# Kernel optimization log

Measured on AMD Instinct MI355X. Metric: run time of the kernel, lower is better.

Reference implementation:

```python
import jax, jax.numpy as jnp
import numpy as np

N_HEAD = 12
M_HIST = 5      # Anderson history window (AndersonAcceleration.m)
BETA = 1.0      # Anderson mixing (AndersonAcceleration.beta)
LN_EPS = 1e-5


def _layer_norm(x, w, b):
    mu = x.mean(-1, keepdims=True)
    xc = x - mu
    var = (xc * xc).mean(-1, keepdims=True)
    return xc * jax.lax.rsqrt(var + LN_EPS) * w + b


def _mha(x, wqkv, bqkv, wo, bo):
    # torch nn.MultiheadAttention, batch_first, self-attention, no mask, dropout=0
    B, T, C = x.shape
    dh = C // N_HEAD
    qkv = x @ wqkv.T + bqkv                       # [B,T,3C]
    q, k, v = jnp.split(qkv, 3, axis=-1)
    def heads(t):
        return t.reshape(B, T, N_HEAD, dh).transpose(0, 2, 1, 3)  # [B,H,T,dh]
    q, k, v = heads(q), heads(k), heads(v)
    scores = jnp.einsum('bhqd,bhkd->bhqk', q, k) / jnp.sqrt(jnp.asarray(dh, x.dtype))
    att = jax.nn.softmax(scores, axis=-1)
    out = jnp.einsum('bhqk,bhkd->bhqd', att, v).transpose(0, 2, 1, 3).reshape(B, T, C)
    return out @ wo.T + bo


def _deq_delta(z, u, emb_row, ln1_w, ln1_b, in_proj_w, in_proj_b, out_proj_w,
               out_proj_b, ln2_w, ln2_b, mlp_w1, mlp_b1, mlp_w2, mlp_b2):
    # DEQOperator.forward -> delta_z
    z_temporal = z + 0.1 * emb_row                 # broadcast [C] over [B,T,C]
    z_ctx = z_temporal + u
    x = _layer_norm(z_ctx, ln1_w, ln1_b)
    attn_out = _mha(x, in_proj_w, in_proj_b, out_proj_w, out_proj_b)
    z_attn = z + attn_out
    h = _layer_norm(z_attn, ln2_w, ln2_b)
    h = jax.nn.gelu(h @ mlp_w1.T + mlp_b1, approximate=False) @ mlp_w2.T + mlp_b2
    z_mlp = z_attn + h
    return z_mlp - z


def _deq_solve(u, iter_emb, ln1_w, ln1_b, in_proj_w, in_proj_b, out_proj_w,
               out_proj_b, ln2_w, ln2_b, mlp_w1, mlp_b1, mlp_w2, mlp_b2, num_iters):
    B, T, C = u.shape
    z = jnp.zeros_like(u)
    Xs, Fs = [], []   # Anderson history of states / residuals
    max_row = iter_emb.shape[0] - 1
    for it in range(num_iters):
        emb_row = iter_emb[min(it, max_row)]
        delta = _deq_delta(z, u, emb_row, ln1_w, ln1_b, in_proj_w, in_proj_b,
                           out_proj_w, out_proj_b, ln2_w, ln2_b,
                           mlp_w1, mlp_b1, mlp_w2, mlp_b2)
        res = delta  # residual of f(z) = z + delta_z w.r.t. z
        Xs.append(z); Fs.append(res)
        if len(Xs) > M_HIST:
            Xs.pop(0); Fs.pop(0)
        if len(Xs) == 1:
            z = z + BETA * res
        else:
            K = len(Xs) - 1
            dF = jnp.stack(Fs[:-1], 0) - res[None]               # [K,B,T,C]
            dF_f = dF.transpose(1, 2, 0, 3).reshape(B * T, K, C)  # per-token LS
            r_f = res.reshape(B * T, C)
            G = jnp.einsum('nkc,nlc->nkl', dF_f, dF_f)            # [BT,K,K]
            G = G + 1e-6 * jnp.eye(K, dtype=u.dtype)
            bvec = jnp.einsum('nkc,nc->nk', dF_f, r_f)            # [BT,K]
            alpha = jnp.linalg.solve(G, bvec[..., None])[..., 0]
            d = r_f - jnp.einsum('nkc,nk->nc', dF_f, alpha)
            z = (z.reshape(B * T, C) + BETA * d).reshape(B, T, C)
    return z


def setup_inputs() -> dict:
    key = jax.random.key(0)
    ks = jax.random.split(key, 6)
    B, T, C = 4, 1024, 768
    std = 0.02
    return {
        'u': jax.random.normal(ks[0], (B, T, C), jnp.float32),
        'iter_emb': std * jax.random.normal(ks[1], (31, C), jnp.float32),
        'ln1_w': jnp.ones((C,), jnp.float32),
        'ln1_b': jnp.zeros((C,), jnp.float32),
        'in_proj_w': std * jax.random.normal(ks[2], (3 * C, C), jnp.float32),
        'in_proj_b': jnp.zeros((3 * C,), jnp.float32),
        'out_proj_w': std * jax.random.normal(ks[3], (C, C), jnp.float32),
        'out_proj_b': jnp.zeros((C,), jnp.float32),
        'ln2_w': jnp.ones((C,), jnp.float32),
        'ln2_b': jnp.zeros((C,), jnp.float32),
        'mlp_w1': std * jax.random.normal(ks[4], (4 * C, C), jnp.float32),
        'mlp_b1': jnp.zeros((4 * C,), jnp.float32),
        'mlp_w2': std * jax.random.normal(ks[5], (C, 4 * C), jnp.float32),
        'mlp_b2': jnp.zeros((C,), jnp.float32),
        'num_iters': 6,
    }


def reference(u, iter_emb, ln1_w, ln1_b, in_proj_w, in_proj_b, out_proj_w,
              out_proj_b, ln2_w, ln2_b, mlp_w1, mlp_b1, mlp_w2, mlp_b2, num_iters):
    return _deq_solve(u, iter_emb, ln1_w, ln1_b, in_proj_w, in_proj_b,
                      out_proj_w, out_proj_b, ln2_w, ln2_b,
                      mlp_w1, mlp_b1, mlp_w2, mlp_b2, int(num_iters))
```

## Files before the change

kernel.cpp:

```cpp
#include <hip/hip_runtime.h>
#include <math.h>

#define BT 4096
#define CDIM 768
#define NHEAD 12
#define DH 64
#define TSEQ 1024
#define BBATCH 4

typedef _Float16 f16;
typedef __attribute__((ext_vector_type(4))) _Float16 f16x4;
typedef __attribute__((ext_vector_type(8))) _Float16 f16x8;
typedef __attribute__((ext_vector_type(4))) float f32x4;

typedef const __attribute__((address_space(1))) unsigned int* gas1_t;
typedef __attribute__((address_space(3))) unsigned int* las3_t;
__device__ __forceinline__ void glds16(const void* g, void* l) {
  __builtin_amdgcn_global_load_lds((gas1_t)g, (las3_t)l, 16, 0, 0);
}

__device__ __forceinline__ float block_reduce_sum(float v, float* sbuf) {
#pragma unroll
  for (int o = 32; o > 0; o >>= 1) v += __shfl_down(v, o, 64);
  int lane = threadIdx.x & 63;
  int w = threadIdx.x >> 6;
  if (lane == 0) sbuf[w] = v;
  __syncthreads();
  float r = sbuf[0] + sbuf[1] + sbuf[2] + sbuf[3];
  __syncthreads();
  return r;
}

__global__ __launch_bounds__(256) void zero_kernel(float4* __restrict__ p) {
  p[(size_t)blockIdx.x * 256 + threadIdx.x] = make_float4(0.f, 0.f, 0.f, 0.f);
}

__global__ __launch_bounds__(256) void cvt_f16_kernel(
    const float* __restrict__ in, f16* __restrict__ out) {
  size_t i = ((size_t)blockIdx.x * 256 + threadIdx.x) * 4;
  float4 v = *(const float4*)(in + i);
  f16x4 o = {(f16)v.x, (f16)v.y, (f16)v.z, (f16)v.w};
  *(f16x4*)(out + i) = o;
}

__global__ __launch_bounds__(256) void ln1_kernel(
    const float* __restrict__ z, const float* __restrict__ u,
    const float* __restrict__ emb, const float* __restrict__ w,
    const float* __restrict__ b, f16* __restrict__ x) {
  __shared__ float sbuf[4];
  int row = blockIdx.x;
  int tid = threadIdx.x;
  const float* zr = z + (size_t)row * CDIM;
  const float* ur = u + (size_t)row * CDIM;
  float v[3];
  float s = 0.f;
#pragma unroll
  for (int i = 0; i < 3; i++) {
    int c = tid + i * 256;
    v[i] = zr[c] + 0.1f * emb[c] + ur[c];
    s += v[i];
  }
  s = block_reduce_sum(s, sbuf);
  float mu = s * (1.f / CDIM);
  float sq = 0.f;
#pragma unroll
  for (int i = 0; i < 3; i++) { v[i] -= mu; sq += v[i] * v[i]; }
  sq = block_reduce_sum(sq, sbuf);
  float rstd = rsqrtf(sq * (1.f / CDIM) + 1e-5f);
  f16* xr = x + (size_t)row * CDIM;
#pragma unroll
  for (int i = 0; i < 3; i++) {
    int c = tid + i * 256;
    xr[c] = (f16)(v[i] * rstd * w[c] + b[c]);
  }
}

__global__ __launch_bounds__(256) void ln2_kernel(
    const float* __restrict__ in, const float* __restrict__ w,
    const float* __restrict__ b, f16* __restrict__ x,
    const float* __restrict__ z, const float* __restrict__ b2,
    float* __restrict__ rinit) {
  __shared__ float sbuf[4];
  int row = blockIdx.x;
  int tid = threadIdx.x;
  const float* ir = in + (size_t)row * CDIM;
  const float* zr = z + (size_t)row * CDIM;
  float* rr = rinit + (size_t)row * CDIM;
  float v[3];
  float s = 0.f;
#pragma unroll
  for (int i = 0; i < 3; i++) {
    int c = tid + i * 256;
    v[i] = ir[c];
    rr[c] = v[i] - zr[c] + b2[c];
    s += v[i];
  }
  s = block_reduce_sum(s, sbuf);
  float mu = s * (1.f / CDIM);
  float sq = 0.f;
#pragma unroll
  for (int i = 0; i < 3; i++) { v[i] -= mu; sq += v[i] * v[i]; }
  sq = block_reduce_sum(sq, sbuf);
  float rstd = rsqrtf(sq * (1.f / CDIM) + 1e-5f);
  f16* xr = x + (size_t)row * CDIM;
#pragma unroll
  for (int i = 0; i < 3; i++) {
    int c = tid + i * 256;
    xr[c] = (f16)(v[i] * rstd * w[c] + b[c]);
  }
}

__device__ __forceinline__ float gelu_exact(float t) {
  return 0.5f * t * (1.f + erff(t * 0.70710678118654752f));
}

template <int MODE>
__global__ __launch_bounds__(256, 3) void gemm_mfma(
    const f16* __restrict__ A, const f16* __restrict__ W,
    const float* __restrict__ bias, f16* __restrict__ hq,
    f16* __restrict__ hk, f16* __restrict__ hvt, f16* __restrict__ hout,
    int M, int N, int K) {
  __shared__ __align__(16) f16 As[128 * 64];
  __shared__ __align__(16) f16 Bs[128 * 64];
  int tid = threadIdx.x;
  int wv = tid >> 6, lane = tid & 63;
  int bm = blockIdx.y, bn = blockIdx.x;
  int wm = (wv >> 1) * 64, wn = (wv & 1) * 64;

  int srow = wv * 32 + (lane >> 3);
  int scole = 8 * ((lane & 7) ^ (lane >> 3));
  const f16* gA = A + (size_t)(bm * 128 + srow) * K + scole;
  const f16* gB = W + (size_t)(bn * 128 + srow) * K + scole;

  f32x4 acc[4][4];
#pragma unroll
  for (int i = 0; i < 4; i++)
#pragma unroll
    for (int j = 0; j < 4; j++) acc[i][j] = (f32x4){0.f, 0.f, 0.f, 0.f};

  int am = lane & 15;
  int quad = lane >> 4;
  int sx = am & 7;

  for (int k0 = 0; k0 < K; k0 += 64) {
    __syncthreads();
#pragma unroll
    for (int j = 0; j < 4; j++) {
      glds16(gA + (size_t)(j * 8) * K + k0, &As[(wv * 32 + j * 8) * 64]);
      glds16(gB + (size_t)(j * 8) * K + k0, &Bs[(wv * 32 + j * 8) * 64]);
    }
    __syncthreads();
#pragma unroll
    for (int kk = 0; kk < 2; kk++) {
      int ce = 8 * (((kk << 2) + quad) ^ sx);
      f16x8 af[4], bfr[4];
#pragma unroll
      for (int mi = 0; mi < 4; mi++)
        af[mi] = *(const f16x8*)&As[(wm + mi * 16 + am) * 64 + ce];
#pragma unroll
      for (int nj = 0; nj < 4; nj++)
        bfr[nj] = *(const f16x8*)&Bs[(wn + nj * 16 + am) * 64 + ce];
#pragma unroll
      for (int mi = 0; mi < 4; mi++)
#pragma unroll
        for (int nj = 0; nj < 4; nj++)
          acc[mi][nj] = __builtin_amdgcn_mfma_f32_16x16x32_f16(
              af[mi], bfr[nj], acc[mi][nj], 0, 0, 0);
    }
  }

  int crow0 = bm * 128 + wm + quad * 4;
  int ccol0 = bn * 128 + wn + am;
#pragma unroll
  for (int nj = 0; nj < 4; nj++) {
    int col = ccol0 + nj * 16;
    float bcol = bias[col];
    if constexpr (MODE == 3) {
      int which = col / CDIM;
      int rem = col - which * CDIM;
      int h = rem >> 6;
      int d = rem & 63;
#pragma unroll
      for (int mi = 0; mi < 4; mi++) {
#pragma unroll
        for (int r = 0; r < 4; r++) {
          int m = crow0 + mi * 16 + r;
          int bb = m >> 10, t = m & 1023;
          f16 val = (f16)(acc[mi][nj][r] + bcol);
          if (which == 0)
            hq[(((size_t)(bb * NHEAD + h) * TSEQ + t) << 6) + d] = val;
          else if (which == 1)
            hk[(((size_t)(bb * NHEAD + h) * TSEQ + t) << 6) + d] = val;
          else
            hvt[(((size_t)(bb * NHEAD + h) * DH + d) << 10) + t] = val;
        }
      }
    } else {
#pragma unroll
      for (int mi = 0; mi < 4; mi++) {
#pragma unroll
        for (int r = 0; r < 4; r++) {
          int m = crow0 + mi * 16 + r;
          size_t idx = (size_t)m * N + col;
          hout[idx] = (f16)gelu_exact(acc[mi][nj][r] + bcol);
        }
      }
    }
  }
}

#define GS 72
template <int MODE>
__global__ __launch_bounds__(256, (MODE == 4) ? 6 : 4) void gemm_mfma64(
    const f16* __restrict__ A, const f16* __restrict__ W,
    const float* __restrict__ bias, const float* __restrict__ aux1,
    float* __restrict__ fout0, int M, int N, int K) {
  __shared__ __align__(16) f16 As[64 * GS];
  __shared__ __align__(16) f16 Bs[64 * GS];
  int tid = threadIdx.x;
  int wv = tid >> 6, lane = tid & 63;
  int bm = blockIdx.x, bn = blockIdx.y;
  int wm = (wv >> 1) * 32, wn = (wv & 1) * 32;

  int ks = (MODE == 4) ? blockIdx.z : 0;
  int kl = (MODE == 4) ? (K >> 1) : K;

  int srow = tid >> 2;
  int scol = (tid & 3) * 16;
  const f16* gA = A + (size_t)(bm * 64 + srow) * K + ks * kl + scol;
  const f16* gB = W + (size_t)(bn * 64 + srow) * K + ks * kl + scol;

  f32x4 acc[2][2];
#pragma unroll
  for (int i = 0; i < 2; i++)
#pragma unroll
    for (int j = 0; j < 2; j++) acc[i][j] = (f32x4){0.f, 0.f, 0.f, 0.f};

  int am = lane & 15;
  int ak = (lane >> 4) * 8;

  f16x8 a0 = *(const f16x8*)(gA);
  f16x8 a1 = *(const f16x8*)(gA + 8);
  f16x8 b0 = *(const f16x8*)(gB);
  f16x8 b1 = *(const f16x8*)(gB + 8);

  for (int k0 = 0; k0 < kl; k0 += 64) {
    __syncthreads();
    *(f16x8*)&As[srow * GS + scol] = a0;
    *(f16x8*)&As[srow * GS + scol + 8] = a1;
    *(f16x8*)&Bs[srow * GS + scol] = b0;
    *(f16x8*)&Bs[srow * GS + scol + 8] = b1;
    __syncthreads();
    int kn = k0 + 64;
    if (kn < kl) {
      a0 = *(const f16x8*)(gA + kn);
      a1 = *(const f16x8*)(gA + kn + 8);
      b0 = *(const f16x8*)(gB + kn);
      b1 = *(const f16x8*)(gB + kn + 8);
    }
#pragma unroll
    for (int kk = 0; kk < 2; kk++) {
      f16x8 af[2], bfr[2];
#pragma unroll
      for (int mi = 0; mi < 2; mi++)
        af[mi] = *(const f16x8*)&As[(wm + mi * 16 + am) * GS + kk * 32 + ak];
#pragma unroll
      for (int nj = 0; nj < 2; nj++)
        bfr[nj] = *(const f16x8*)&Bs[(wn + nj * 16 + am) * GS + kk * 32 + ak];
#pragma unroll
      for (int mi = 0; mi < 2; mi++)
#pragma unroll
        for (int nj = 0; nj < 2; nj++)
          acc[mi][nj] = __builtin_amdgcn_mfma_f32_16x16x32_f16(
              af[mi], bfr[nj], acc[mi][nj], 0, 0, 0);
    }
  }

  int crow0 = bm * 64 + wm + (lane >> 4) * 4;
  int ccol0 = bn * 64 + wn + (lane & 15);
#pragma unroll
  for (int nj = 0; nj < 2; nj++) {
    int col = ccol0 + nj * 16;
    float bcol = (MODE == 4) ? 0.f : bias[col];
#pragma unroll
    for (int mi = 0; mi < 2; mi++) {
#pragma unroll
      for (int r = 0; r < 4; r++) {
        int m = crow0 + mi * 16 + r;
        size_t idx = (size_t)m * N + col;
        if constexpr (MODE == 0) {
          fout0[idx] = acc[mi][nj][r] + bcol + aux1[idx];
        } else {
          unsafeAtomicAdd(fout0 + idx, acc[mi][nj][r]);
        }
      }
    }
  }
}

#define PSTRIDE 72
#define KVS 72
__global__ __launch_bounds__(256, 3) void flash_attn8(
    const f16* __restrict__ Qg, const f16* __restrict__ Kg,
    const f16* __restrict__ Vt, f16* __restrict__ attn) {
  __shared__ __align__(16) f16 Ks[64 * KVS];
  __shared__ __align__(16) f16 Vs[64 * KVS];
  __shared__ __align__(16) f16 Plds[4][16 * PSTRIDE];
  int tid = threadIdx.x;
  int wv = tid >> 6, lane = tid & 63;
  int bh = blockIdx.x;
  int bb = bh / NHEAD, h = bh % NHEAD;
  int m0 = (blockIdx.y * 4 + wv) * 16;
  int am = lane & 15;
  int quad = lane >> 4;
  int ak = quad * 8;

  int srow = tid >> 3;
  int scol = (tid & 7) * 8;

  const f16* kb = Kg + (((size_t)bh * TSEQ) << 6);
  const f16* vb = Vt + (((size_t)bh * DH) << 10);

  const f16* qbase = Qg + (((size_t)bh * TSEQ + m0) << 6);
  f16x8 qf0 = *(const f16x8*)(qbase + am * 64 + ak);
  f16x8 qf1 = *(const f16x8*)(qbase + am * 64 + 32 + ak);
#pragma unroll
  for (int i = 0; i < 8; i++) { qf0[i] *= (f16)0.125f; qf1[i] *= (f16)0.125f; }

  f16* Pw = Plds[wv];
  f32x4 Oa[4];
#pragma unroll
  for (int i = 0; i < 4; i++) Oa[i] = (f32x4){0.f, 0.f, 0.f, 0.f};
  float lpart[4] = {0.f, 0.f, 0.f, 0.f};

  f16x8 kr0 = *(const f16x8*)(kb + (size_t)srow * 64 + scol);
  f16x8 kr1 = *(const f16x8*)(kb + (size_t)(32 + srow) * 64 + scol);
  f16x8 vr0 = *(const f16x8*)(vb + (size_t)srow * TSEQ + scol);
  f16x8 vr1 = *(const f16x8*)(vb + (size_t)(32 + srow) * TSEQ + scol);

  for (int n0 = 0; n0 < TSEQ; n0 += 64) {
    __syncthreads();
    *(f16x8*)&Ks[srow * KVS + scol] = kr0;
    *(f16x8*)&Ks[(32 + srow) * KVS + scol] = kr1;
    *(f16x8*)&Vs[srow * KVS + scol] = vr0;
    *(f16x8*)&Vs[(32 + srow) * KVS + scol] = vr1;
    __syncthreads();
    int nn = n0 + 64;
    if (nn < TSEQ) {
      kr0 = *(const f16x8*)(kb + (size_t)(nn + srow) * 64 + scol);
      kr1 = *(const f16x8*)(kb + (size_t)(nn + 32 + srow) * 64 + scol);
      vr0 = *(const f16x8*)(vb + (size_t)srow * TSEQ + nn + scol);
      vr1 = *(const f16x8*)(vb + (size_t)(32 + srow) * TSEQ + nn + scol);
    }
    f32x4 S[4];
#pragma unroll
    for (int t = 0; t < 4; t++) {
      f16x8 kf0 = *(const f16x8*)&Ks[(16 * t + am) * KVS + ak];
      f16x8 kf1 = *(const f16x8*)&Ks[(16 * t + am) * KVS + 32 + ak];
      S[t] = __builtin_amdgcn_mfma_f32_16x16x32_f16(
          qf0, kf0, (f32x4){0.f, 0.f, 0.f, 0.f}, 0, 0, 0);
      S[t] = __builtin_amdgcn_mfma_f32_16x16x32_f16(qf1, kf1, S[t], 0, 0, 0);
    }
#pragma unroll
    for (int t = 0; t < 4; t++) {
#pragma unroll
      for (int r = 0; r < 4; r++) {
        float p = __expf(S[t][r]);
        lpart[r] += p;
        Pw[(quad * 4 + r) * PSTRIDE + 16 * t + am] = (f16)p;
      }
    }
    f16x8 pa0 = *(const f16x8*)&Pw[am * PSTRIDE + ak];
    f16x8 pa1 = *(const f16x8*)&Pw[am * PSTRIDE + 32 + ak];
#pragma unroll
    for (int dt = 0; dt < 4; dt++) {
      f16x8 vf0 = *(const f16x8*)&Vs[(16 * dt + am) * KVS + ak];
      f16x8 vf1 = *(const f16x8*)&Vs[(16 * dt + am) * KVS + 32 + ak];
      Oa[dt] = __builtin_amdgcn_mfma_f32_16x16x32_f16(pa0, vf0, Oa[dt], 0, 0, 0);
      Oa[dt] = __builtin_amdgcn_mfma_f32_16x16x32_f16(pa1, vf1, Oa[dt], 0, 0, 0);
    }
  }

#pragma unroll
  for (int o = 1; o < 16; o <<= 1)
#pragma unroll
    for (int r = 0; r < 4; r++) lpart[r] += __shfl_xor(lpart[r], o, 64);

#pragma unroll
  for (int r = 0; r < 4; r++) {
    int m = m0 + quad * 4 + r;
    float inv = 1.f / lpart[r];
    f16* orow = attn + ((size_t)(bb * TSEQ + m)) * CDIM + h * DH;
#pragma unroll
    for (int dt = 0; dt < 4; dt++)
      orow[dt * 16 + am] = (f16)(Oa[dt][r] * inv);
  }
}

template <int KA>
__global__ __launch_bounds__(256) void anderson_ln1(
    float* __restrict__ z, const float* __restrict__ rescur,
    const float* __restrict__ p0, const float* __restrict__ p1,
    const float* __restrict__ p2, const float* __restrict__ p3,
    const float* __restrict__ u, const float* __restrict__ emb,
    const float* __restrict__ w, const float* __restrict__ b,
    f16* __restrict__ x) {
  __shared__ float sbuf[4];
  int row = blockIdx.x, tid = threadIdx.x;
  size_t base = (size_t)row * CDIM + tid;
  float r[3];
#pragma unroll
  for (int i = 0; i < 3; i++) r[i] = rescur[base + i * 256];

  float zn[3];
  if constexpr (KA == 0) {
#pragma unroll
    for (int i = 0; i < 3; i++) zn[i] = z[base + i * 256] + r[i];
  } else {
    const float* ps[4] = {p0, p1, p2, p3};
    float dF[KA == 0 ? 1 : KA][3];
#pragma unroll
    for (int k = 0; k < KA; k++)
#pragma unroll
      for (int i = 0; i < 3; i++) dF[k][i] = ps[k][base + i * 256] - r[i];

    float Gm[KA == 0 ? 1 : KA][KA == 0 ? 1 : KA], bv[KA == 0 ? 1 : KA];
#pragma unroll
    for (int k = 0; k < KA; k++) {
#pragma unroll
      for (int ll = k; ll < KA; ll++) {
        float p = 0.f;
#pragma unroll
        for (int i = 0; i < 3; i++) p += dF[k][i] * dF[ll][i];
        float t = block_reduce_sum(p, sbuf);
        Gm[k][ll] = t;
        Gm[ll][k] = t;
      }
    }
#pragma unroll
    for (int k = 0; k < KA; k++) Gm[k][k] += 1e-6f;
#pragma unroll
    for (int k = 0; k < KA; k++) {
      float p = 0.f;
#pragma unroll
      for (int i = 0; i < 3; i++) p += dF[k][i] * r[i];
      bv[k] = block_reduce_sum(p, sbuf);
    }
    float alpha[KA == 0 ? 1 : KA];
#pragma unroll
    for (int p = 0; p < KA; p++) {
      float inv = 1.f / Gm[p][p];
#pragma unroll
      for (int rr = p + 1; rr < KA; rr++) {
        float f = Gm[rr][p] * inv;
#pragma unroll
        for (int c = p; c < KA; c++) Gm[rr][c] -= f * Gm[p][c];
        bv[rr] -= f * bv[p];
      }
    }
#pragma unroll
    for (int p = KA - 1; p >= 0; p--) {
      float s2 = bv[p];
#pragma unroll
      for (int c = p + 1; c < KA; c++) s2 -= Gm[p][c] * alpha[c];
      alpha[p] = s2 / Gm[p][p];
    }
#pragma unroll
    for (int i = 0; i < 3; i++) {
      float d = r[i];
#pragma unroll
      for (int k = 0; k < KA; k++) d = fmaf(-dF[k][i], alpha[k], d);
      zn[i] = z[base + i * 256] + d;
    }
  }
#pragma unroll
  for (int i = 0; i < 3; i++) z[base + i * 256] = zn[i];

  const float* ur = u + (size_t)row * CDIM;
  float v[3];
  float s = 0.f;
#pragma unroll
  for (int i = 0; i < 3; i++) {
    int c = tid + i * 256;
    v[i] = zn[i] + 0.1f * emb[c] + ur[c];
    s += v[i];
  }
  s = block_reduce_sum(s, sbuf);
  float mu = s * (1.f / CDIM);
  float sq = 0.f;
#pragma unroll
  for (int i = 0; i < 3; i++) { v[i] -= mu; sq += v[i] * v[i]; }
  sq = block_reduce_sum(sq, sbuf);
  float rstd = rsqrtf(sq * (1.f / CDIM) + 1e-5f);
  f16* xr = x + (size_t)row * CDIM;
#pragma unroll
  for (int i = 0; i < 3; i++) {
    int c = tid + i * 256;
    xr[c] = (f16)(v[i] * rstd * w[c] + b[c]);
  }
}

template <int KA>
__global__ __launch_bounds__(256) void anderson_kernel(
    float* __restrict__ z, const float* __restrict__ rescur,
    const float* __restrict__ p0, const float* __restrict__ p1,
    const float* __restrict__ p2, const float* __restrict__ p3) {
  __shared__ float sbuf[4];
  int row = blockIdx.x, tid = threadIdx.x;
  size_t base = (size_t)row * CDIM + tid;
  float r[3];
#pragma unroll
  for (int i = 0; i < 3; i++) r[i] = rescur[base + i * 256];
  const float* ps[4] = {p0, p1, p2, p3};
  float dF[KA][3];
#pragma unroll
  for (int k = 0; k < KA; k++)
#pragma unroll
    for (int i = 0; i < 3; i++) dF[k][i] = ps[k][base + i * 256] - r[i];

  float Gm[KA][KA], bv[KA];
#pragma unroll
  for (int k = 0; k < KA; k++) {
#pragma unroll
    for (int ll = k; ll < KA; ll++) {
      float p = 0.f;
#pragma unroll
      for (int i = 0; i < 3; i++) p += dF[k][i] * dF[ll][i];
      float t = block_reduce_sum(p, sbuf);
      Gm[k][ll] = t;
      Gm[ll][k] = t;
    }
  }
#pragma unroll
  for (int k = 0; k < KA; k++) Gm[k][k] += 1e-6f;
#pragma unroll
  for (int k = 0; k < KA; k++) {
    float p = 0.f;
#pragma unroll
    for (int i = 0; i < 3; i++) p += dF[k][i] * r[i];
    bv[k] = block_reduce_sum(p, sbuf);
  }
  float alpha[KA];
#pragma unroll
  for (int p = 0; p < KA; p++) {
    float inv = 1.f / Gm[p][p];
#pragma unroll
    for (int rr = p + 1; rr < KA; rr++) {
      float f = Gm[rr][p] * inv;
#pragma unroll
      for (int c = p; c < KA; c++) Gm[rr][c] -= f * Gm[p][c];
      bv[rr] -= f * bv[p];
    }
  }
#pragma unroll
  for (int p = KA - 1; p >= 0; p--) {
    float s2 = bv[p];
#pragma unroll
    for (int c = p + 1; c < KA; c++) s2 -= Gm[p][c] * alpha[c];
    alpha[p] = s2 / Gm[p][p];
  }
#pragma unroll
  for (int i = 0; i < 3; i++) {
    float d = r[i];
#pragma unroll
    for (int k = 0; k < KA; k++) d = fmaf(-dF[k][i], alpha[k], d);
    z[base + i * 256] += d;
  }
}

extern "C" void kernel_launch(void* const* d_in, const int* in_sizes, int n_in,
                              void* d_out, int out_size, void* d_ws,
                              size_t ws_size, hipStream_t stream) {
  (void)in_sizes; (void)n_in; (void)out_size; (void)ws_size;
  const float* u = (const float*)d_in[0];
  const float* iter_emb = (const float*)d_in[1];
  const float* ln1w = (const float*)d_in[2];
  const float* ln1b = (const float*)d_in[3];
  const float* wqkv = (const float*)d_in[4];
  const float* bqkv = (const float*)d_in[5];
  const float* wo = (const float*)d_in[6];
  const float* bo = (const float*)d_in[7];
  const float* ln2w = (const float*)d_in[8];
  const float* ln2b = (const float*)d_in[9];
  const float* w1 = (const float*)d_in[10];
  const float* b1 = (const float*)d_in[11];
  const float* w2 = (const float*)d_in[12];
  const float* b2 = (const float*)d_in[13];

  const size_t S = (size_t)BT * CDIM;
  float* ws = (float*)d_ws;
  float* z = ws + 0 * S;
  float* zattn = ws + 1 * S;
  float* res[5] = {ws + 2 * S, ws + 3 * S, ws + 4 * S, ws + 5 * S, ws + 6 * S};
  f16* q_h = (f16*)(ws + 7 * S);
  f16* k_h = q_h + S;
  f16* vt_h = q_h + 2 * S;
  f16* h_h = (f16*)(ws + 7 * S);
  f16* x_h = (f16*)(ws + 9 * S);
  f16* wqkv_h = x_h + S;
  f16* wo_h = wqkv_h + (size_t)3 * CDIM * CDIM;
  f16* w1_h = wo_h + (size_t)CDIM * CDIM;
  f16* w2_h = w1_h + (size_t)4 * CDIM * CDIM;

  cvt_f16_kernel<<<1728, 256, 0, stream>>>(wqkv, wqkv_h);
  cvt_f16_kernel<<<576, 256, 0, stream>>>(wo, wo_h);
  cvt_f16_kernel<<<2304, 256, 0, stream>>>(w1, w1_h);
  cvt_f16_kernel<<<2304, 256, 0, stream>>>(w2, w2_h);
  zero_kernel<<<S / 1024, 256, 0, stream>>>((float4*)z);

  for (int it = 0; it < 6; it++) {
    float* rcur = res[it % 5];
    if (it == 0) {
      ln1_kernel<<<BT, 256, 0, stream>>>(z, u, iter_emb, ln1w, ln1b, x_h);
    }
    gemm_mfma<3><<<dim3(18, 32), 256, 0, stream>>>(
        x_h, wqkv_h, bqkv, q_h, k_h, vt_h, nullptr, BT, 3 * CDIM, CDIM);
    flash_attn8<<<dim3(BBATCH * NHEAD, TSEQ / 64), 256, 0, stream>>>(
        q_h, k_h, vt_h, x_h);
    gemm_mfma64<0><<<dim3(64, 12), 256, 0, stream>>>(
        x_h, wo_h, bo, z, zattn, BT, CDIM, CDIM);
    ln2_kernel<<<BT, 256, 0, stream>>>(zattn, ln2w, ln2b, x_h, z, b2, rcur);
    gemm_mfma<1><<<dim3(24, 32), 256, 0, stream>>>(
        x_h, w1_h, b1, nullptr, nullptr, nullptr, h_h, BT, 4 * CDIM, CDIM);
    gemm_mfma64<4><<<dim3(64, 12, 2), 256, 0, stream>>>(
        h_h, w2_h, b2, nullptr, rcur, BT, CDIM, 4 * CDIM);

    int Kh = it < 4 ? it : 4;
    const float* p[4] = {rcur, rcur, rcur, rcur};
    for (int kx = 1; kx <= Kh; kx++) p[kx - 1] = res[(it - kx) % 5];
    if (it < 5) {
      const float* embn = iter_emb + (it + 1) * CDIM;
      switch (Kh) {
        case 0: anderson_ln1<0><<<BT, 256, 0, stream>>>(z, rcur, p[0], p[1], p[2], p[3], u, embn, ln1w, ln1b, x_h); break;
        case 1: anderson_ln1<1><<<BT, 256, 0, stream>>>(z, rcur, p[0], p[1], p[2], p[3], u, embn, ln1w, ln1b, x_h); break;
        case 2: anderson_ln1<2><<<BT, 256, 0, stream>>>(z, rcur, p[0], p[1], p[2], p[3], u, embn, ln1w, ln1b, x_h); break;
        case 3: anderson_ln1<3><<<BT, 256, 0, stream>>>(z, rcur, p[0], p[1], p[2], p[3], u, embn, ln1w, ln1b, x_h); break;
        default: anderson_ln1<4><<<BT, 256, 0, stream>>>(z, rcur, p[0], p[1], p[2], p[3], u, embn, ln1w, ln1b, x_h); break;
      }
    } else {
      anderson_kernel<4><<<BT, 256, 0, stream>>>(z, rcur, p[0], p[1], p[2], p[3]);
    }
  }
  hipMemcpyAsync(d_out, z, S * sizeof(float), hipMemcpyDeviceToDevice, stream);
}
```

Before: 1.150 ms.

## Replace MLP down-projection with 128x128 split-K GEMM using direct global-to-LDS loads

```diff
diff --git a/kernel.cpp b/kernel.cpp
--- a/kernel.cpp
+++ b/kernel.cpp
@@ -209,9 +209,83 @@
   }
 }
 
+#define KCHUNK 768
+__global__ __launch_bounds__(256, 3) void gemm_splitk_glds(
+    const f16* __restrict__ A, const f16* __restrict__ W,
+    float* __restrict__ out, int N, int Ktot) {
+  __shared__ __align__(16) f16 As[128 * 64];
+  __shared__ __align__(16) f16 Bs[128 * 64];
+  int b = blockIdx.x;
+  int n = (b & 7) * 96 + (b >> 3);
+  int bn = n % 6;
+  int bm = (n / 6) & 31;
+  int ks = n / 192;
+
+  int tid = threadIdx.x;
+  int wv = tid >> 6, lane = tid & 63;
+  int wm = (wv >> 1) * 64, wn = (wv & 1) * 64;
+
+  int srow = wv * 32 + (lane >> 3);
+  int scole = 8 * ((lane & 7) ^ (lane >> 3));
+  const f16* gA = A + (size_t)(bm * 128 + srow) * Ktot + ks * KCHUNK + scole;
+  const f16* gB = W + (size_t)(bn * 128 + srow) * Ktot + ks * KCHUNK + scole;
+
+  f32x4 acc[4][4];
+#pragma unroll
+  for (int i = 0; i < 4; i++)
+#pragma unroll
+    for (int j = 0; j < 4; j++) acc[i][j] = (f32x4){0.f, 0.f, 0.f, 0.f};
+
+  int am = lane & 15;
+  int quad = lane >> 4;
+  int sx = am & 7;
+
+  for (int k0 = 0; k0 < KCHUNK; k0 += 64) {
+    __syncthreads();
+#pragma unroll
+    for (int j = 0; j < 4; j++) {
+      glds16(gA + (size_t)(j * 8) * Ktot + k0, &As[(wv * 32 + j * 8) * 64]);
+      glds16(gB + (size_t)(j * 8) * Ktot + k0, &Bs[(wv * 32 + j * 8) * 64]);
+    }
+    __syncthreads();
+#pragma unroll
+    for (int kk = 0; kk < 2; kk++) {
+      int ce = 8 * (((kk << 2) + quad) ^ sx);
+      f16x8 af[4], bfr[4];
+#pragma unroll
+      for (int mi = 0; mi < 4; mi++)
+        af[mi] = *(const f16x8*)&As[(wm + mi * 16 + am) * 64 + ce];
+#pragma unroll
+      for (int nj = 0; nj < 4; nj++)
+        bfr[nj] = *(const f16x8*)&Bs[(wn + nj * 16 + am) * 64 + ce];
+#pragma unroll
+      for (int mi = 0; mi < 4; mi++)
+#pragma unroll
+        for (int nj = 0; nj < 4; nj++)
+          acc[mi][nj] = __builtin_amdgcn_mfma_f32_16x16x32_f16(
+              af[mi], bfr[nj], acc[mi][nj], 0, 0, 0);
+    }
+  }
+
+  int crow0 = bm * 128 + wm + quad * 4;
+  int ccol0 = bn * 128 + wn + am;
+#pragma unroll
+  for (int nj = 0; nj < 4; nj++) {
+    int col = ccol0 + nj * 16;
+#pragma unroll
+    for (int mi = 0; mi < 4; mi++) {
+#pragma unroll
+      for (int r = 0; r < 4; r++) {
+        int m = crow0 + mi * 16 + r;
+        unsafeAtomicAdd(out + (size_t)m * N + col, acc[mi][nj][r]);
+      }
+    }
+  }
+}
+
 #define GS 72
 template <int MODE>
-__global__ __launch_bounds__(256, (MODE == 4) ? 6 : 4) void gemm_mfma64(
+__global__ __launch_bounds__(256, 4) void gemm_mfma64(
     const f16* __restrict__ A, const f16* __restrict__ W,
     const float* __restrict__ bias, const float* __restrict__ aux1,
     float* __restrict__ fout0, int M, int N, int K) {
@@ -222,13 +296,10 @@
   int bm = blockIdx.x, bn = blockIdx.y;
   int wm = (wv >> 1) * 32, wn = (wv & 1) * 32;
 
-  int ks = (MODE == 4) ? blockIdx.z : 0;
-  int kl = (MODE == 4) ? (K >> 1) : K;
-
   int srow = tid >> 2;
   int scol = (tid & 3) * 16;
-  const f16* gA = A + (size_t)(bm * 64 + srow) * K + ks * kl + scol;
-  const f16* gB = W + (size_t)(bn * 64 + srow) * K + ks * kl + scol;
+  const f16* gA = A + (size_t)(bm * 64 + srow) * K + scol;
+  const f16* gB = W + (size_t)(bn * 64 + srow) * K + scol;
 
   f32x4 acc[2][2];
 #pragma unroll
@@ -244,7 +315,7 @@
   f16x8 b0 = *(const f16x8*)(gB);
   f16x8 b1 = *(const f16x8*)(gB + 8);
 
-  for (int k0 = 0; k0 < kl; k0 += 64) {
+  for (int k0 = 0; k0 < K; k0 += 64) {
     __syncthreads();
     *(f16x8*)&As[srow * GS + scol] = a0;
     *(f16x8*)&As[srow * GS + scol + 8] = a1;
@@ -252,7 +323,7 @@
     *(f16x8*)&Bs[srow * GS + scol + 8] = b1;
     __syncthreads();
     int kn = k0 + 64;
-    if (kn < kl) {
+    if (kn < K) {
       a0 = *(const f16x8*)(gA + kn);
       a1 = *(const f16x8*)(gA + kn + 8);
       b0 = *(const f16x8*)(gB + kn);
@@ -281,18 +352,14 @@
 #pragma unroll
   for (int nj = 0; nj < 2; nj++) {
     int col = ccol0 + nj * 16;
-    float bcol = (MODE == 4) ? 0.f : bias[col];
+    float bcol = bias[col];
 #pragma unroll
     for (int mi = 0; mi < 2; mi++) {
 #pragma unroll
       for (int r = 0; r < 4; r++) {
         int m = crow0 + mi * 16 + r;
         size_t idx = (size_t)m * N + col;
-        if constexpr (MODE == 0) {
-          fout0[idx] = acc[mi][nj][r] + bcol + aux1[idx];
-        } else {
-          unsafeAtomicAdd(fout0 + idx, acc[mi][nj][r]);
-        }
+        fout0[idx] = acc[mi][nj][r] + bcol + aux1[idx];
       }
     }
   }
@@ -622,8 +689,8 @@
     ln2_kernel<<<BT, 256, 0, stream>>>(zattn, ln2w, ln2b, x_h, z, b2, rcur);
     gemm_mfma<1><<<dim3(24, 32), 256, 0, stream>>>(
         x_h, w1_h, b1, nullptr, nullptr, nullptr, h_h, BT, 4 * CDIM, CDIM);
-    gemm_mfma64<4><<<dim3(64, 12, 2), 256, 0, stream>>>(
-        h_h, w2_h, b2, nullptr, rcur, BT, CDIM, 4 * CDIM);
+    gemm_splitk_glds<<<dim3(768), 256, 0, stream>>>(
+        h_h, w2_h, rcur, CDIM, 4 * CDIM);
 
     int Kh = it < 4 ? it : 4;
     const float* p[4] = {rcur, rcur, rcur, rcur};
```

New measurement: 1.260 ms. 9.6% more time.
